# Performance work log

Measured on AMD Instinct MI355X. Metric: run time of the kernel, lower is better.

## Reference

```python
import jax, jax.numpy as jnp
import numpy as np


def setup_inputs() -> dict:
    key = jax.random.key(0)
    ks = jax.random.split(key, 8)
    B, Cin, Cattr, Cout, H, W = 8, 256, 256, 256, 64, 64
    x = jax.random.normal(ks[0], (B, Cin, H, W), dtype=jnp.float32)
    attr = jax.random.normal(ks[1], (B, Cattr, H, W), dtype=jnp.float32)
    # 1x1 conv weights stored as [out, in] (kernel_size=1 squeezed)
    sq = 1.0 / np.sqrt(Cin)
    sa = 1.0 / np.sqrt(Cattr)
    Wq = jax.random.uniform(ks[2], (Cout, Cin), jnp.float32, -sq, sq)
    bq = jax.random.uniform(ks[3], (Cout,), jnp.float32, -sq, sq)
    Wk = jax.random.uniform(ks[4], (Cout, Cattr), jnp.float32, -sa, sa)
    bk = jax.random.uniform(ks[5], (Cout,), jnp.float32, -sa, sa)
    Wv = jax.random.uniform(ks[6], (Cout, Cattr), jnp.float32, -sa, sa)
    bv = jax.random.uniform(ks[7], (Cout,), jnp.float32, -sa, sa)
    return {"x": x, "attr": attr, "Wq": Wq, "bq": bq, "Wk": Wk, "bk": bk, "Wv": Wv, "bv": bv}


def reference(x, attr, Wq, bq, Wk, bk, Wv, bv):
    B, Cin, H, W = x.shape
    # 1x1 convs == per-pixel linear projections
    q = jnp.einsum('bchw,oc->bohw', x, Wq) + bq[None, :, None, None]      # [B,C,H,W]
    k = jnp.einsum('bchw,oc->bohw', attr, Wk) + bk[None, :, None, None]
    v = jnp.einsum('bchw,oc->bohw', attr, Wv) + bv[None, :, None, None]
    C = q.shape[1]
    qf = q.reshape(B, C, H * W)   # [B,C,N]
    kf = k.reshape(B, C, H * W)
    vf = v.reshape(B, C, H * W)
    # attn[b,i,j] = sum_c q[b,c,i] * k[b,c,j]  -> softmax over j
    attn = jax.nn.softmax(jnp.einsum('bci,bcj->bij', qf, kf), axis=-1)    # [B,N,N]
    out = jnp.einsum('bcj,bij->bci', vf, attn)                            # [B,C,N]
    return out.reshape(B, C, H, W) + x
```

## Files before the change

### kernel.cpp

```cpp
#include <hip/hip_runtime.h>

typedef _Float16 f16;
typedef _Float16 f16x8 __attribute__((ext_vector_type(8)));
typedef _Float16 f16x4 __attribute__((ext_vector_type(4)));
typedef float f32x4 __attribute__((ext_vector_type(4)));
typedef float f32x16 __attribute__((ext_vector_type(16)));

#define LOG2E 1.44269504088896340736f
#define SOFF  36.0f
#define CDIM 256
#define NPIX 4096

__device__ __forceinline__ void gl2lds16(const f16* g, const f16* l) {
    __builtin_amdgcn_global_load_lds((const __attribute__((address_space(1))) unsigned int*)g,
                                     (__attribute__((address_space(3))) unsigned int*)l, 16, 0, 0);
}

__global__ void convert_w_kernel(const float* __restrict__ Wq, const float* __restrict__ Wk,
                                 const float* __restrict__ Wv,
                                 f16* __restrict__ WqF, f16* __restrict__ WkF,
                                 f16* __restrict__ WvF) {
    int t = blockIdx.x * 256 + threadIdx.x;
    int m = t >> 13;
    int g = t & 8191;
    int lane = g & 63;
    int ksct = g >> 6;
    int ks = ksct & 15, ct = ksct >> 4;
    int o = ct * 32 + (lane & 31);
    int cin0 = ks * 16 + (lane >> 5) * 8;
    const float* W = (m == 0) ? Wq : ((m == 1) ? Wk : Wv);
    f16* WF = (m == 0) ? WqF : ((m == 1) ? WkF : WvF);
    const float scale = (m == 0) ? LOG2E : 1.0f;
    const float* src = W + (size_t)o * CDIM + cin0;
    f16x8 v;
#pragma unroll
    for (int e = 0; e < 8; ++e) v[e] = (f16)(src[e] * scale);
    *(f16x8*)(WF + (size_t)g * 8) = v;
}

__global__ __launch_bounds__(256, 2)
void proj_kernel(const float* __restrict__ x, const float* __restrict__ attr,
                 const f16* __restrict__ WqF, const float* __restrict__ bq,
                 const f16* __restrict__ WkF, const float* __restrict__ bk,
                 const f16* __restrict__ WvF, const float* __restrict__ bv,
                 f16* __restrict__ qT, f16* __restrict__ kT, f16* __restrict__ vW) {
    __shared__ __align__(16) f16 Xs[64 * 256];
    __shared__ __align__(16) f16 As[64 * 256];
    __shared__ __align__(16) f16 Ostage[4][1024];

    const int b  = blockIdx.x & 7;
    const int i0 = (blockIdx.x >> 3) * 64;
    const int t  = threadIdx.x;
    const int w = t >> 6, lane = t & 63, l31 = lane & 31, hi = lane >> 5;
    const int xu  = (l31 >> 1) & 15;
    const int hib = (hi ^ (l31 & 1)) * 8;

    {
        const int i  = t & 63;
        const int cb = t >> 6;
        const float* xb = x    + (size_t)b * CDIM * NPIX + i0 + i;
        const float* ab = attr + (size_t)b * CDIM * NPIX + i0 + i;
#pragma unroll 2
        for (int rep = 0; rep < 8; ++rep) {
            int chunk = cb * 8 + rep;
            const float* xs = xb + (size_t)(chunk * 8) * NPIX;
            const float* as_ = ab + (size_t)(chunk * 8) * NPIX;
            f16x8 xv, av;
#pragma unroll
            for (int e = 0; e < 8; ++e) {
                xv[e] = (f16)xs[(size_t)e * NPIX];
                av[e] = (f16)as_[(size_t)e * NPIX];
            }
            int phys = chunk ^ (i & 31);
            *(f16x8*)(Xs + i * 256 + phys * 8) = xv;
            *(f16x8*)(As + i * 256 + phys * 8) = av;
        }
    }
    __syncthreads();

#pragma unroll 1
    for (int k = 0; k < 12; ++k) {
        const int tt = w + 4 * k;
        const int kind = tt >> 4;
        const int rr = tt & 15;
        const int ct = rr >> 1;
        const int half = rr & 1;

        const f16* WF = (kind == 0) ? WqF : ((kind == 1) ? WkF : WvF);
        const f16* Bs = (kind == 0) ? Xs : As;
        const float* bias = (kind == 0) ? bq : ((kind == 1) ? bk : bv);
        const float bscale = (kind == 0) ? LOG2E : 1.0f;

        const f16* ap = WF + (size_t)(ct * 16) * 512 + (size_t)lane * 8;
        const f16* bp = Bs + (half * 32 + l31) * 256 + hib;

        f32x16 acc;
#pragma unroll
        for (int r = 0; r < 16; ++r) acc[r] = 0.0f;
#pragma unroll
        for (int ks = 0; ks < 16; ++ks) {
            f16x8 afr = *(const f16x8*)(ap + ks * 512);
            f16x8 bfr = *(const f16x8*)(bp + ((ks ^ xu) << 4));
            acc = __builtin_amdgcn_mfma_f32_32x32x16_f16(afr, bfr, acc, 0, 0, 0);
        }

        f16* st = Ostage[w];
        if (kind < 2) {
#pragma unroll
            for (int g = 0; g < 4; ++g) {
                f32x4 bb = *(const f32x4*)(bias + ct * 32 + 4 * hi + 8 * g);
                f16x4 pk;
#pragma unroll
                for (int e = 0; e < 4; ++e) pk[e] = (f16)(acc[4 * g + e] + bb[e] * bscale);
                *(f16x4*)(st + l31 * 32 + 4 * hi + 8 * g) = pk;
            }
            f16* dst = ((kind == 0) ? qT : kT)
                       + ((size_t)b * NPIX + i0 + half * 32) * CDIM + ct * 32;
#pragma unroll
            for (int d = 0; d < 2; ++d) {
                int row = d * 16 + (lane >> 2);
                int c8  = (lane & 3) * 8;
                f16x8 v = *(const f16x8*)(st + row * 32 + c8);
                *(f16x8*)(dst + (size_t)row * CDIM + c8) = v;
            }
        } else {
#pragma unroll
            for (int g = 0; g < 4; ++g) {
                f32x4 bb = *(const f32x4*)(bias + ct * 32 + 4 * hi + 8 * g);
#pragma unroll
                for (int e = 0; e < 4; ++e) {
                    int c31 = 4 * hi + 8 * g + e;
                    st[c31 * 32 + l31] = (f16)(acc[4 * g + e] + bb[e]);
                }
            }
            const int j0 = i0 + half * 32;
            f16* dstb = vW + (size_t)b * CDIM * NPIX + (size_t)(ct * 32) * NPIX + j0;
#pragma unroll
            for (int d = 0; d < 2; ++d) {
                int chunk = d * 64 + lane;
                int c31 = chunk >> 2, jch = chunk & 3;
                *(f16x8*)(dstb + (size_t)c31 * NPIX + jch * 8) =
                    *(const f16x8*)(st + chunk * 8);
            }
        }
    }
}

__global__ __launch_bounds__(512, 2)
void attn_kernel(const f16* __restrict__ qT, const f16* __restrict__ kT,
                 const f16* __restrict__ vW, const float* __restrict__ x,
                 float* __restrict__ out) {
    extern __shared__ unsigned char smem[];

    const int b    = blockIdx.x & 7;
    const int i0   = (blockIdx.x >> 3) * 128;
    const int t    = threadIdx.x;
    const int w    = t >> 6;
    const int lane = t & 63;
    const int l31  = lane & 31;
    const int hi   = lane >> 5;
    const int iw   = (w & 3) * 32;
    const int jh   = (w >> 2) * 32;
    const int jh8  = (w >> 2) * 4;
    const int ig   = i0 + iw + l31;
    const int xorv = l31 & 7;

    f16x8 qf[16];
    {
        const f16* qp = qT + ((size_t)b * NPIX + ig) * CDIM + hi * 8;
#pragma unroll
        for (int ks = 0; ks < 16; ++ks) qf[ks] = *(const f16x8*)(qp + ks * 16);
    }

    int kp4o[4];
    {
        int kboff = (jh + l31) * 256 + (hi ^ (xorv & 1)) * 8;
        const int xv2 = xorv >> 1;
#pragma unroll
        for (int r = 0; r < 4; ++r) kp4o[r] = kboff + (r ^ xv2) * 16;
    }
    int vp2o[2];
    {
        int vbase = 16384 + (l31 >> 2) * 256 + (l31 & 3) * 64;
#pragma unroll
        for (int kj = 0; kj < 2; ++kj)
            vp2o[kj] = vbase + (((jh8 + 2 * kj + hi) ^ (l31 & 7))) * 8;
    }

    f32x16 acc[8];
#pragma unroll
    for (int ct = 0; ct < 8; ++ct)
#pragma unroll
        for (int r = 0; r < 16; ++r) acc[ct][r] = 0.0f;
    float lrun = 0.0f;

    const f16* kb = kT + (size_t)b * NPIX * CDIM;
    const f16* vb = vW + (size_t)b * CDIM * NPIX;
    f16* lds0 = (f16*)smem;
    const int wub = (t & ~63) * 8;

    {
#pragma unroll
        for (int rep = 0; rep < 4; ++rep) {
            int slot = t + rep * 512;
            int krow = slot >> 5, kpc = slot & 31;
            gl2lds16(kb + (size_t)krow * CDIM + ((kpc ^ (krow & 7)) * 8),
                     lds0 + wub + rep * 4096);
            int R = slot >> 5, pv = slot & 31;
            int vc = 4 * R + (pv >> 3);
            int vjc = (pv & 7) ^ (vc & 7);
            gl2lds16(vb + (size_t)vc * NPIX + vjc * 8,
                     lds0 + 16384 + wub + rep * 4096);
        }
    }

    union Q4 { f16x4 h; unsigned int u[2]; };
    union B8 { f16x8 h; unsigned int u[4]; };

#pragma unroll 1
    for (int jt = 0; jt < 64; ++jt) {
        const int p = jt & 1;
        __syncthreads();

        if (jt < 63) {
            const int j0n = (jt + 1) * 64;
            f16* dstb = lds0 + (p ^ 1) * 32768;
#pragma unroll
            for (int rep = 0; rep < 4; ++rep) {
                int slot = t + rep * 512;
                int krow = slot >> 5, kpc = slot & 31;
                gl2lds16(kb + (size_t)(j0n + krow) * CDIM + ((kpc ^ (krow & 7)) * 8),
                         dstb + wub + rep * 4096);
                int R = slot >> 5, pv = slot & 31;
                int vc = 4 * R + (pv >> 3);
                int vjc = (pv & 7) ^ (vc & 7);
                gl2lds16(vb + (size_t)vc * NPIX + j0n + vjc * 8,
                         dstb + 16384 + wub + rep * 4096);
            }
        }

        const f16* L = lds0 + p * 32768;

        f32x16 s;
#pragma unroll
        for (int r = 0; r < 16; ++r) s[r] = -SOFF;
#pragma unroll
        for (int ks = 0; ks < 16; ++ks)
            s = __builtin_amdgcn_mfma_f32_32x32x16_f16(
                *(const f16x8*)(L + kp4o[ks & 3] + (ks >> 2) * 64), qf[ks], s, 0, 0, 0);

        Q4 ownq[4];
        float rtot = 0.0f;
#pragma unroll
        for (int g = 0; g < 4; ++g) {
            float p0 = __builtin_amdgcn_exp2f(s[4 * g + 0]);
            float p1 = __builtin_amdgcn_exp2f(s[4 * g + 1]);
            float p2 = __builtin_amdgcn_exp2f(s[4 * g + 2]);
            float p3 = __builtin_amdgcn_exp2f(s[4 * g + 3]);
            rtot += (p0 + p1) + (p2 + p3);
            ownq[g].h[0] = (f16)p0; ownq[g].h[1] = (f16)p1;
            ownq[g].h[2] = (f16)p2; ownq[g].h[3] = (f16)p3;
        }
        lrun += rtot;

        f16x8 pb[2];
#pragma unroll
        for (int kj = 0; kj < 2; ++kj) {
            int sidx = 2 * kj + 1 - hi;
            int oidx = 2 * kj + hi;
            unsigned int s0 = ownq[sidx].u[0], s1 = ownq[sidx].u[1];
            unsigned int r0 = (unsigned int)__shfl_xor((int)s0, 32);
            unsigned int r1 = (unsigned int)__shfl_xor((int)s1, 32);
            B8 bb;
            bb.u[0] = hi ? r0 : ownq[oidx].u[0];
            bb.u[1] = hi ? r1 : ownq[oidx].u[1];
            bb.u[2] = hi ? ownq[oidx].u[0] : r0;
            bb.u[3] = hi ? ownq[oidx].u[1] : r1;
            pb[kj] = bb.h;
        }

#pragma unroll
        for (int ct = 0; ct < 8; ++ct) {
            acc[ct] = __builtin_amdgcn_mfma_f32_32x32x16_f16(
                *(const f16x8*)(L + vp2o[0] + ct * 2048), pb[0], acc[ct], 0, 0, 0);
            acc[ct] = __builtin_amdgcn_mfma_f32_32x32x16_f16(
                *(const f16x8*)(L + vp2o[1] + ct * 2048), pb[1], acc[ct], 0, 0, 0);
        }
    }

    float lsum = lrun + __shfl_xor(lrun, 32);
    __syncthreads();
    float* Obuf = (float*)smem;
    float* Ls   = (float*)(smem + 131072);
    if (w >= 4) {
        float* ob = Obuf + (w - 4) * 8192;
#pragma unroll
        for (int ct = 0; ct < 8; ++ct)
#pragma unroll
            for (int r = 0; r < 16; ++r) {
                int c = ct * 32 + (r & 3) + 8 * (r >> 2) + 4 * hi;
                ob[c * 32 + l31] = acc[ct][r];
            }
        if (hi == 0) Ls[(w - 4) * 32 + l31] = lsum;
    }
    __syncthreads();
    if (w < 4) {
        const float ltot = lsum + Ls[w * 32 + l31];
        const float invl = 1.0f / ltot;
        const float* po = Obuf + w * 8192;
        const float* xb = x + (size_t)b * CDIM * NPIX + i0 + iw;
        float* og = out + (size_t)b * CDIM * NPIX + i0 + iw;
#pragma unroll
        for (int ct = 0; ct < 8; ++ct)
#pragma unroll
            for (int r = 0; r < 16; ++r) {
                int c = ct * 32 + (r & 3) + 8 * (r >> 2) + 4 * hi;
                size_t off = (size_t)c * NPIX + l31;
                og[off] = (acc[ct][r] + po[c * 32 + l31]) * invl + xb[off];
            }
    }
}

extern "C" void kernel_launch(void* const* d_in, const int* in_sizes, int n_in,
                              void* d_out, int out_size, void* d_ws, size_t ws_size,
                              hipStream_t stream) {
    const float* x    = (const float*)d_in[0];
    const float* attr = (const float*)d_in[1];
    const float* Wq   = (const float*)d_in[2];
    const float* bq   = (const float*)d_in[3];
    const float* Wk   = (const float*)d_in[4];
    const float* bk   = (const float*)d_in[5];
    const float* Wv   = (const float*)d_in[6];
    const float* bv   = (const float*)d_in[7];
    float* out = (float*)d_out;

    char* ws = (char*)d_ws;
    const size_t qkv_bytes = (size_t)8 * NPIX * CDIM * sizeof(f16);
    f16* qT   = (f16*)ws;
    f16* kT   = (f16*)(ws + qkv_bytes);
    f16* vW   = (f16*)(ws + 2 * qkv_bytes);
    f16* WqF  = (f16*)(ws + 3 * qkv_bytes);
    f16* WkF  = WqF + 65536;
    f16* WvF  = WkF + 65536;

    (void)hipFuncSetAttribute((const void*)attn_kernel,
                              hipFuncAttributeMaxDynamicSharedMemorySize, 131584);

    convert_w_kernel<<<96, 256, 0, stream>>>(Wq, Wk, Wv, WqF, WkF, WvF);
    proj_kernel<<<512, 256, 0, stream>>>(x, attr, WqF, bq, WkF, bk, WvF, bv, qT, kT, vW);
    attn_kernel<<<256, 512, 131584, stream>>>(qT, kT, vW, x, out);
}
```

Measured before the change: 298.5 us.

## Store K in channel-chunked layout and remap K/V LDS tiles for conflict-free reads

The projection kernel now writes K as [b][channel-group-of-8][pixel][8] chunks instead of pixel-major rows. This lets the attention kernel load K tiles with contiguous 16-byte chunks and read MFMA operands with a simple linear LDS offset rather than XOR-swizzled addressing. The V tile's LDS mapping and read offsets are also reorganised. The goal is to cut address arithmetic and LDS bank conflicts in the inner loop. The risk is a less coalesced scatter when proj_kernel writes K.

New measurement: 296.1 us. About the same (-0.8%).

```diff
diff --git a/kernel.cpp b/kernel.cpp
--- a/kernel.cpp
+++ b/kernel.cpp
@@ -43,7 +43,7 @@
                  const f16* __restrict__ WqF, const float* __restrict__ bq,
                  const f16* __restrict__ WkF, const float* __restrict__ bk,
                  const f16* __restrict__ WvF, const float* __restrict__ bv,
-                 f16* __restrict__ qT, f16* __restrict__ kT, f16* __restrict__ vW) {
+                 f16* __restrict__ qT, f16* __restrict__ kC, f16* __restrict__ vW) {
     __shared__ __align__(16) f16 Xs[64 * 256];
     __shared__ __align__(16) f16 As[64 * 256];
     __shared__ __align__(16) f16 Ostage[4][1024];
@@ -114,14 +114,25 @@
                 for (int e = 0; e < 4; ++e) pk[e] = (f16)(acc[4 * g + e] + bb[e] * bscale);
                 *(f16x4*)(st + l31 * 32 + 4 * hi + 8 * g) = pk;
             }
-            f16* dst = ((kind == 0) ? qT : kT)
-                       + ((size_t)b * NPIX + i0 + half * 32) * CDIM + ct * 32;
-#pragma unroll
-            for (int d = 0; d < 2; ++d) {
-                int row = d * 16 + (lane >> 2);
-                int c8  = (lane & 3) * 8;
-                f16x8 v = *(const f16x8*)(st + row * 32 + c8);
-                *(f16x8*)(dst + (size_t)row * CDIM + c8) = v;
+            if (kind == 0) {
+                f16* dst = qT + ((size_t)b * NPIX + i0 + half * 32) * CDIM + ct * 32;
+#pragma unroll
+                for (int d = 0; d < 2; ++d) {
+                    int row = d * 16 + (lane >> 2);
+                    int c8  = (lane & 3) * 8;
+                    f16x8 v = *(const f16x8*)(st + row * 32 + c8);
+                    *(f16x8*)(dst + (size_t)row * CDIM + c8) = v;
+                }
+            } else {
+                const int j0 = i0 + half * 32;
+                f16* dstb = kC + (size_t)b * CDIM * NPIX;
+#pragma unroll
+                for (int d = 0; d < 2; ++d) {
+                    int row = d * 16 + (lane >> 2);
+                    int kl  = lane & 3;
+                    f16x8 v = *(const f16x8*)(st + row * 32 + kl * 8);
+                    *(f16x8*)(dstb + ((size_t)(ct * 4 + kl) * NPIX + j0 + row) * 8) = v;
+                }
             }
         } else {
 #pragma unroll
@@ -147,7 +158,7 @@
 }
 
 __global__ __launch_bounds__(512, 2)
-void attn_kernel(const f16* __restrict__ qT, const f16* __restrict__ kT,
+void attn_kernel(const f16* __restrict__ qT, const f16* __restrict__ kC,
                  const f16* __restrict__ vW, const float* __restrict__ x,
                  float* __restrict__ out) {
     extern __shared__ unsigned char smem[];
@@ -163,7 +174,6 @@
     const int jh   = (w >> 2) * 32;
     const int jh8  = (w >> 2) * 4;
     const int ig   = i0 + iw + l31;
-    const int xorv = l31 & 7;
 
     f16x8 qf[16];
     {
@@ -172,19 +182,13 @@
         for (int ks = 0; ks < 16; ++ks) qf[ks] = *(const f16x8*)(qp + ks * 16);
     }
 
-    int kp4o[4];
-    {
-        int kboff = (jh + l31) * 256 + (hi ^ (xorv & 1)) * 8;
-        const int xv2 = xorv >> 1;
-#pragma unroll
-        for (int r = 0; r < 4; ++r) kp4o[r] = kboff + (r ^ xv2) * 16;
-    }
+    const int kbase = hi * 512 + (jh >> 5) * 256 + l31 * 8;
     int vp2o[2];
     {
-        int vbase = 16384 + (l31 >> 2) * 256 + (l31 & 3) * 64;
+        int vbase = 16384 + (l31 & 7) * 256 + ((l31 >> 3) << 6);
 #pragma unroll
         for (int kj = 0; kj < 2; ++kj)
-            vp2o[kj] = vbase + (((jh8 + 2 * kj + hi) ^ (l31 & 7))) * 8;
+            vp2o[kj] = vbase + (((jh8 + 2 * kj + hi) ^ (l31 & 7)) << 3);
     }
 
     f32x16 acc[8];
@@ -194,7 +198,7 @@
         for (int r = 0; r < 16; ++r) acc[ct][r] = 0.0f;
     float lrun = 0.0f;
 
-    const f16* kb = kT + (size_t)b * NPIX * CDIM;
+    const f16* kb = kC + (size_t)b * CDIM * NPIX;
     const f16* vb = vW + (size_t)b * CDIM * NPIX;
     f16* lds0 = (f16*)smem;
     const int wub = (t & ~63) * 8;
@@ -203,12 +207,12 @@
 #pragma unroll
         for (int rep = 0; rep < 4; ++rep) {
             int slot = t + rep * 512;
-            int krow = slot >> 5, kpc = slot & 31;
-            gl2lds16(kb + (size_t)krow * CDIM + ((kpc ^ (krow & 7)) * 8),
+            int kc = slot >> 6, jhalf = (slot >> 5) & 1, pj = slot & 31;
+            gl2lds16(kb + ((size_t)kc * NPIX + jhalf * 32 + pj) * 8,
                      lds0 + wub + rep * 4096);
-            int R = slot >> 5, pv = slot & 31;
-            int vc = 4 * R + (pv >> 3);
-            int vjc = (pv & 7) ^ (vc & 7);
+            int row = slot >> 5, pv = slot & 31;
+            int vc = ((row >> 3) << 5) | (((pv >> 3) & 3) << 3) | (row & 7);
+            int vjc = (pv & 7) ^ (row & 7);
             gl2lds16(vb + (size_t)vc * NPIX + vjc * 8,
                      lds0 + 16384 + wub + rep * 4096);
         }
@@ -228,12 +232,12 @@
 #pragma unroll
             for (int rep = 0; rep < 4; ++rep) {
                 int slot = t + rep * 512;
-                int krow = slot >> 5, kpc = slot & 31;
-                gl2lds16(kb + (size_t)(j0n + krow) * CDIM + ((kpc ^ (krow & 7)) * 8),
+                int kc = slot >> 6, jhalf = (slot >> 5) & 1, pj = slot & 31;
+                gl2lds16(kb + ((size_t)kc * NPIX + j0n + jhalf * 32 + pj) * 8,
                          dstb + wub + rep * 4096);
-                int R = slot >> 5, pv = slot & 31;
-                int vc = 4 * R + (pv >> 3);
-                int vjc = (pv & 7) ^ (vc & 7);
+                int row = slot >> 5, pv = slot & 31;
+                int vc = ((row >> 3) << 5) | (((pv >> 3) & 3) << 3) | (row & 7);
+                int vjc = (pv & 7) ^ (row & 7);
                 gl2lds16(vb + (size_t)vc * NPIX + j0n + vjc * 8,
                          dstb + 16384 + wub + rep * 4096);
             }
@@ -247,7 +251,7 @@
 #pragma unroll
         for (int ks = 0; ks < 16; ++ks)
             s = __builtin_amdgcn_mfma_f32_32x32x16_f16(
-                *(const f16x8*)(L + kp4o[ks & 3] + (ks >> 2) * 64), qf[ks], s, 0, 0, 0);
+                *(const f16x8*)(L + kbase + ks * 1024), qf[ks], s, 0, 0, 0);
 
         Q4 ownq[4];
         float rtot = 0.0f;
@@ -337,7 +341,7 @@
     char* ws = (char*)d_ws;
     const size_t qkv_bytes = (size_t)8 * NPIX * CDIM * sizeof(f16);
     f16* qT   = (f16*)ws;
-    f16* kT   = (f16*)(ws + qkv_bytes);
+    f16* kC   = (f16*)(ws + qkv_bytes);
     f16* vW   = (f16*)(ws + 2 * qkv_bytes);
     f16* WqF  = (f16*)(ws + 3 * qkv_bytes);
     f16* WkF  = WqF + 65536;
@@ -347,6 +351,6 @@
                               hipFuncAttributeMaxDynamicSharedMemorySize, 131584);
 
     convert_w_kernel<<<96, 256, 0, stream>>>(Wq, Wk, Wv, WqF, WkF, WvF);
-    proj_kernel<<<512, 256, 0, stream>>>(x, attr, WqF, bq, WkF, bk, WvF, bv, qT, kT, vW);
-    attn_kernel<<<256, 512, 131584, stream>>>(qT, kT, vW, x, out);
-}
+    proj_kernel<<<512, 256, 0, stream>>>(x, attr, WqF, bq, WkF, bk, WvF, bv, qT, kC, vW);
+    attn_kernel<<<256, 512, 131584, stream>>>(qT, kC, vW, x, out);
+}
```
